# Kernel optimization log

Measured on AMD Instinct MI355X. Metric: run time of the kernel, lower is better.

Reference implementation:

```python
import jax, jax.numpy as jnp
import numpy as np

B, T, E, H, C = 64, 512, 768, 128, 18


def setup_inputs() -> dict:
    key = jax.random.key(0)
    ks = jax.random.split(key, 16)
    s = 1.0 / np.sqrt(H)
    inp = {
        "x": jax.random.normal(ks[0], (B, T, E), jnp.float32),
        "attention_mask": jnp.ones((B, T), jnp.int32),
        "labels": jax.random.randint(ks[1], (B, T), 0, C, jnp.int32),
        "Wih_f": jax.random.uniform(ks[2], (4 * H, E), jnp.float32, -s, s),
        "Whh_f": jax.random.uniform(ks[3], (4 * H, H), jnp.float32, -s, s),
        "b_f": jax.random.uniform(ks[4], (4 * H,), jnp.float32, -s, s),
        "Wih_b": jax.random.uniform(ks[5], (4 * H, E), jnp.float32, -s, s),
        "Whh_b": jax.random.uniform(ks[6], (4 * H, H), jnp.float32, -s, s),
        "b_b": jax.random.uniform(ks[7], (4 * H,), jnp.float32, -s, s),
        "Wfc": jax.random.uniform(ks[8], (C, 2 * H), jnp.float32, -s, s),
        "bfc": jax.random.uniform(ks[9], (C,), jnp.float32, -s, s),
        "start_trans": jax.random.normal(ks[10], (C,), jnp.float32) * 0.1,
        "end_trans": jax.random.normal(ks[11], (C,), jnp.float32) * 0.1,
        "trans": jax.random.normal(ks[12], (C, C), jnp.float32) * 0.1,
    }
    return inp


def _lstm_dir(x, Wih, Whh, b, reverse=False):
    # x: [B, T, E] -> hidden states [B, T, H]; torch LSTM gate order i,f,g,o
    if reverse:
        x = x[:, ::-1]
    pre = jnp.einsum("bte,ge->btg", x, Wih) + b  # [B, T, 4H] input projection once
    h0 = jnp.zeros((x.shape[0], H), x.dtype)

    def step(carry, pt):
        h, c = carry
        g = pt + h @ Whh.T
        i, f, gg, o = jnp.split(g, 4, axis=-1)
        c = jax.nn.sigmoid(f) * c + jax.nn.sigmoid(i) * jnp.tanh(gg)
        h = jax.nn.sigmoid(o) * jnp.tanh(c)
        return (h, c), h

    _, hs = jax.lax.scan(step, (h0, h0), jnp.swapaxes(pre, 0, 1))
    hs = jnp.swapaxes(hs, 0, 1)
    if reverse:
        hs = hs[:, ::-1]
    return hs


def _crf_loglik(em, tags, mask, start, end, trans):
    # pytorch-crf log-likelihood, batch_first. em [B,T,C], tags/mask [B,T]
    b, t, _ = em.shape
    maskf = mask.astype(em.dtype)
    tags = tags.astype(jnp.int32)
    # numerator: score of the given tag path
    em_sc = jnp.take_along_axis(em, tags[..., None], axis=2)[..., 0]  # [B,T]
    num = start[tags[:, 0]] + em_sc[:, 0]
    num = num + jnp.sum(em_sc[:, 1:] * maskf[:, 1:], axis=1)
    num = num + jnp.sum(trans[tags[:, :-1], tags[:, 1:]] * maskf[:, 1:], axis=1)
    last_idx = jnp.sum(mask.astype(jnp.int32), axis=1) - 1
    last_tags = jnp.take_along_axis(tags, last_idx[:, None], axis=1)[:, 0]
    num = num + end[last_tags]
    # denominator: forward algorithm (logsumexp recurrence over time)
    alpha0 = start + em[:, 0]  # [B,C]

    def step(alpha, inp):
        e_t, m_t = inp
        new = jax.scipy.special.logsumexp(alpha[:, :, None] + trans[None], axis=1) + e_t
        return jnp.where(m_t[:, None], new, alpha), None

    alpha, _ = jax.lax.scan(
        step, alpha0,
        (jnp.swapaxes(em[:, 1:], 0, 1), jnp.swapaxes(mask[:, 1:].astype(bool), 0, 1)),
    )
    den = jax.scipy.special.logsumexp(alpha + end, axis=1)
    return num - den


def _viterbi(em, start, end, trans):
    # em [B,T,C] -> best path [B,T] (full mask)
    s0 = start + em[:, 0]

    def fstep(score, e_t):
        cand = score[:, :, None] + trans[None]  # [B,C,C]
        return jnp.max(cand, axis=1) + e_t, jnp.argmax(cand, axis=1)

    score, bptr = jax.lax.scan(fstep, s0, jnp.swapaxes(em[:, 1:], 0, 1))  # bptr [T-1,B,C]
    last = jnp.argmax(score + end, axis=1)  # [B]

    def bstep(tag, ptr_t):
        prev = jnp.take_along_axis(ptr_t, tag[:, None], axis=1)[:, 0]
        return prev, prev

    _, path = jax.lax.scan(bstep, last, bptr, reverse=True)  # [T-1,B]
    return jnp.concatenate([jnp.swapaxes(path, 0, 1), last[:, None]], axis=1)


def reference(x, attention_mask, labels, Wih_f, Whh_f, b_f, Wih_b, Whh_b, b_b,
              Wfc, bfc, start_trans, end_trans, trans):
    hf = _lstm_dir(x, Wih_f, Whh_f, b_f, reverse=False)
    hb = _lstm_dir(x, Wih_b, Whh_b, b_b, reverse=True)
    seq = jnp.concatenate([hf, hb], axis=-1)  # [B,T,2H]
    em = seq @ Wfc.T + bfc  # [B,T,C] emissions
    mask = attention_mask.astype(bool)
    llh = _crf_loglik(em, labels, mask, start_trans, end_trans, trans)
    loss = -jnp.sum(llh) / x.shape[0]  # reduction='sum' then / batch_size
    path = _viterbi(em, start_trans, end_trans, trans) + 1  # res_paths = x+1
    return path, loss
```

## Files before the change

kernel.cpp:

```cpp
#include <hip/hip_runtime.h>
#include <hip/hip_bf16.h>
#include <math.h>

typedef __attribute__((ext_vector_type(8))) short short8;
typedef __attribute__((ext_vector_type(4))) float f32x4;

constexpr int nB = 64, nT = 512, nE = 768, nH = 128, nG = 512, nC = 18;
constexpr int nBT = nB * nT;

__device__ __forceinline__ float bf2f(unsigned short u) { return __uint_as_float(((unsigned int)u) << 16); }
__device__ __forceinline__ unsigned short f2bf(float f) {
  __hip_bfloat16 h = __float2bfloat16(f);
  return *reinterpret_cast<unsigned short*>(&h);
}
__device__ __forceinline__ float rlane(float v, int lane) {
  return __uint_as_float(__builtin_amdgcn_readlane(__float_as_uint(v), lane));
}
__device__ __forceinline__ float fast_sig(float x) {
  return __builtin_amdgcn_rcpf(1.0f + __builtin_amdgcn_exp2f(-1.44269504f * x));
}
__device__ __forceinline__ float fast_tanh(float x) {
  return 1.0f - 2.0f * __builtin_amdgcn_rcpf(1.0f + __builtin_amdgcn_exp2f(2.88539008f * x));
}
__device__ __forceinline__ float fast_exp(float x) { return __builtin_amdgcn_exp2f(1.44269504f * x); }
__device__ __forceinline__ float fast_log(float x) { return __builtin_amdgcn_logf(x) * 0.69314718f; }

__global__ __launch_bounds__(256) void cvt_kernel(const float* __restrict__ in,
                                                  unsigned short* __restrict__ out, int n8) {
  int i = blockIdx.x * blockDim.x + threadIdx.x;
  const int stride = gridDim.x * blockDim.x;
  for (; i < n8; i += stride) {
    const float4 a = ((const float4*)in)[(size_t)i * 2];
    const float4 b = ((const float4*)in)[(size_t)i * 2 + 1];
    unsigned short u[8] = {f2bf(a.x), f2bf(a.y), f2bf(a.z), f2bf(a.w),
                           f2bf(b.x), f2bf(b.y), f2bf(b.z), f2bf(b.w)};
    ((float4*)out)[i] = *(float4*)u;
  }
}

__global__ __launch_bounds__(256) void proj_kernel(
    const float* __restrict__ x,
    const unsigned short* __restrict__ wfb, const unsigned short* __restrict__ wbb,
    const float* __restrict__ biasF, const float* __restrict__ biasB,
    unsigned short* __restrict__ Pf, unsigned short* __restrict__ Pb)
{
  const int bid = blockIdx.x;
  const int mt = bid & 255, sub = bid >> 8;
  const int dir = sub >> 2, nt = sub & 3;
  const unsigned short* W = dir ? wbb : wfb;
  const float* bias = dir ? biasB : biasF;
  unsigned short* P = dir ? Pb : Pf;
  const int m0 = mt * 128, n0 = nt * 128;

  __shared__ unsigned short As[128 * 40];
  __shared__ unsigned short Bs[128 * 40];
  const int tid = threadIdx.x;
  const int w = tid >> 6, lane = tid & 63, l15 = lane & 15, l4 = lane >> 4;
  const int wr = w >> 1, wc = w & 1;
  const int srow = tid >> 1, shalf = tid & 1;

  const float* srcA = x + (size_t)(m0 + srow) * nE + shalf * 16;
  const unsigned short* srcB = W + (size_t)(n0 + srow) * nE + shalf * 16;

  f32x4 acc[4][4];
#pragma unroll
  for (int i = 0; i < 4; ++i)
#pragma unroll
    for (int j = 0; j < 4; ++j) acc[i][j] = (f32x4){0.f, 0.f, 0.f, 0.f};

  for (int k0 = 0; k0 < nE; k0 += 32) {
    const float4 a0 = *(const float4*)(srcA + k0);
    const float4 a1 = *(const float4*)(srcA + k0 + 4);
    const float4 a2 = *(const float4*)(srcA + k0 + 8);
    const float4 a3 = *(const float4*)(srcA + k0 + 12);
    const float4 b0 = *(const float4*)(srcB + k0);
    const float4 b1 = *(const float4*)(srcB + k0 + 8);
    unsigned short ua[16] = {f2bf(a0.x), f2bf(a0.y), f2bf(a0.z), f2bf(a0.w),
                             f2bf(a1.x), f2bf(a1.y), f2bf(a1.z), f2bf(a1.w),
                             f2bf(a2.x), f2bf(a2.y), f2bf(a2.z), f2bf(a2.w),
                             f2bf(a3.x), f2bf(a3.y), f2bf(a3.z), f2bf(a3.w)};
    __syncthreads();
    *(float4*)&As[srow * 40 + shalf * 16] = *(float4*)&ua[0];
    *(float4*)&As[srow * 40 + shalf * 16 + 8] = *(float4*)&ua[8];
    *(float4*)&Bs[srow * 40 + shalf * 16] = b0;
    *(float4*)&Bs[srow * 40 + shalf * 16 + 8] = b1;
    __syncthreads();
    short8 af[4], bfr[4];
#pragma unroll
    for (int i = 0; i < 4; ++i) af[i] = *(const short8*)&As[(wr * 64 + i * 16 + l15) * 40 + l4 * 8];
#pragma unroll
    for (int j = 0; j < 4; ++j) bfr[j] = *(const short8*)&Bs[(wc * 64 + j * 16 + l15) * 40 + l4 * 8];
#pragma unroll
    for (int i = 0; i < 4; ++i)
#pragma unroll
      for (int j = 0; j < 4; ++j)
        acc[i][j] = __builtin_amdgcn_mfma_f32_16x16x32_bf16(af[i], bfr[j], acc[i][j], 0, 0, 0);
  }
  float bv[4];
#pragma unroll
  for (int j = 0; j < 4; ++j) bv[j] = bias[n0 + wc * 64 + j * 16 + l15];
#pragma unroll
  for (int i = 0; i < 4; ++i) {
#pragma unroll
    for (int j = 0; j < 4; ++j) {
      const int col = n0 + wc * 64 + j * 16 + l15;
#pragma unroll
      for (int r = 0; r < 4; ++r) {
        const int row = m0 + wr * 64 + i * 16 + l4 * 4 + r;
        P[(size_t)row * nG + col] = f2bf(acc[i][j][r] + bv[j]);
      }
    }
  }
}

__global__ __launch_bounds__(512, 1) void lstm_kernel(
    const unsigned short* __restrict__ Pf, const unsigned short* __restrict__ Pb,
    const float* __restrict__ WhhF, const float* __restrict__ WhhB,
    unsigned short* __restrict__ hf, unsigned short* __restrict__ hb)
{
  const int bid = blockIdx.x;
  const int dir = bid & 1, grp = bid >> 1;
  const int b0 = grp * 4;
  const unsigned short* pre = dir ? Pb : Pf;
  const float* Whh = dir ? WhhB : WhhF;
  unsigned short* hout = dir ? hb : hf;

  const int tid = threadIdx.x, w = tid >> 6, lane = tid & 63;
  const int l15 = lane & 15, l4 = lane >> 4;
  const int batch = l15 & 3, msel = l15 >> 2;
  const int cell = w * 16 + msel * 4 + l4;
  const int swz = batch * 40;

  __shared__ unsigned short h_lds[2 * 4 * 128];

  short8 Af[4][4];
#pragma unroll
  for (int m = 0; m < 4; ++m) {
    const int gp = w * 64 + m * 16 + l15;
    const int gorig = (gp & 3) * 128 + (gp >> 2);
#pragma unroll
    for (int kk = 0; kk < 4; ++kk) {
      const float* wp = Whh + (size_t)gorig * nH + kk * 32 + l4 * 8;
      const float4 v0 = *(const float4*)wp;
      const float4 v1 = *(const float4*)(wp + 4);
      unsigned short u[8] = {f2bf(v0.x), f2bf(v0.y), f2bf(v0.z), f2bf(v0.w),
                             f2bf(v1.x), f2bf(v1.y), f2bf(v1.z), f2bf(v1.w)};
      Af[m][kk] = *(short8*)u;
    }
  }
  for (int i = tid; i < 2 * 4 * 128; i += 512) h_lds[i] = 0;

  float c_state = 0.f;
  const unsigned short* pbase = pre + (size_t)(b0 + batch) * nT * nG + cell;

  unsigned short pA[4], pB[4];
  {
    const int tt0 = dir ? (nT - 1) : 0;
    const int tt1 = dir ? (nT - 2) : 1;
#pragma unroll
    for (int r = 0; r < 4; ++r) pA[r] = pbase[(size_t)tt0 * nG + r * 128];
#pragma unroll
    for (int r = 0; r < 4; ++r) pB[r] = pbase[(size_t)tt1 * nG + r * 128];
  }
  __syncthreads();

#define LSTM_STEP(RB, T, BUFC)                                                   \
  {                                                                              \
    const int ttime = dir ? (nT - 1 - (T)) : (T);                                \
    float pg[4];                                                                 \
    _Pragma("unroll")                                                            \
    for (int r = 0; r < 4; ++r) pg[r] = bf2f(BUFC[r]);                           \
    {                                                                            \
      const int tl = ((T) + 2 < nT) ? (T) + 2 : (T);                             \
      const int ttl = dir ? (nT - 1 - tl) : tl;                                  \
      _Pragma("unroll")                                                          \
      for (int r = 0; r < 4; ++r) BUFC[r] = pbase[(size_t)ttl * nG + r * 128];   \
    }                                                                            \
    short8 bfr[4];                                                               \
    _Pragma("unroll")                                                            \
    for (int kk = 0; kk < 4; ++kk) {                                             \
      const int idx = (RB) * 512 + batch * 128 + ((kk * 32 + l4 * 8) ^ swz);     \
      bfr[kk] = *(const short8*)&h_lds[idx];                                     \
    }                                                                            \
    f32x4 acc[4];                                                                \
    _Pragma("unroll")                                                            \
    for (int m = 0; m < 4; ++m) acc[m] = (f32x4){0.f, 0.f, 0.f, 0.f};            \
    _Pragma("unroll")                                                            \
    for (int kk = 0; kk < 4; ++kk)                                               \
      _Pragma("unroll")                                                          \
      for (int m = 0; m < 4; ++m)                                                \
        acc[m] = __builtin_amdgcn_mfma_f32_16x16x32_bf16(Af[m][kk], bfr[kk], acc[m], 0, 0, 0); \
    const float g0 = msel < 2 ? (msel == 0 ? acc[0][0] : acc[1][0]) : (msel == 2 ? acc[2][0] : acc[3][0]); \
    const float g1 = msel < 2 ? (msel == 0 ? acc[0][1] : acc[1][1]) : (msel == 2 ? acc[2][1] : acc[3][1]); \
    const float g2 = msel < 2 ? (msel == 0 ? acc[0][2] : acc[1][2]) : (msel == 2 ? acc[2][2] : acc[3][2]); \
    const float g3 = msel < 2 ? (msel == 0 ? acc[0][3] : acc[1][3]) : (msel == 2 ? acc[2][3] : acc[3][3]); \
    const float gi = g0 + pg[0], gf = g1 + pg[1], gg = g2 + pg[2], go = g3 + pg[3]; \
    c_state = fast_sig(gf) * c_state + fast_sig(gi) * fast_tanh(gg);             \
    const float hval = fast_sig(go) * fast_tanh(c_state);                        \
    const unsigned short hu = f2bf(hval);                                        \
    h_lds[((RB) ^ 1) * 512 + batch * 128 + (cell ^ swz)] = hu;                   \
    hout[((size_t)(b0 + batch) * nT + ttime) * nH + cell] = hu;                  \
    asm volatile("s_waitcnt lgkmcnt(0)" ::: "memory");                           \
    __builtin_amdgcn_sched_barrier(0);                                           \
    __builtin_amdgcn_s_barrier();                                                \
  }

  for (int t2 = 0; t2 < nT; t2 += 2) {
    LSTM_STEP(0, t2, pA)
    LSTM_STEP(1, t2 + 1, pB)
  }
#undef LSTM_STEP
}

__global__ __launch_bounds__(256) void em_kernel(
    const unsigned short* __restrict__ hf, const unsigned short* __restrict__ hb,
    const float* __restrict__ Wfc, const float* __restrict__ bfc,
    float* __restrict__ em)
{
  __shared__ float seq[32][260];
  __shared__ float Wf[18][260];
  const int tid = threadIdx.x;
  const int row0 = blockIdx.x * 32;
  for (int i = tid; i < 32 * 32; i += 256) {
    const int r = i >> 5, seg = i & 31;
    const unsigned short* src = (seg < 16) ? (hf + (size_t)(row0 + r) * nH + seg * 8)
                                           : (hb + (size_t)(row0 + r) * nH + (seg - 16) * 8);
    const float4 v = *(const float4*)src;
    const unsigned short* u = (const unsigned short*)&v;
#pragma unroll
    for (int k = 0; k < 8; ++k) seq[r][seg * 8 + k] = bf2f(u[k]);
  }
  for (int i = tid; i < nC * 256; i += 256) {
    const int cc = i >> 8, k = i & 255;
    Wf[cc][k] = Wfc[cc * 256 + k];
  }
  __syncthreads();
  for (int o = tid; o < 32 * nC; o += 256) {
    const int r = o / nC, cc = o - r * nC;
    float acc = bfc[cc];
    const float4* s4 = (const float4*)&seq[r][0];
    const float4* w4 = (const float4*)&Wf[cc][0];
#pragma unroll
    for (int q = 0; q < 64; ++q) {
      const float4 a = s4[q]; const float4 wv = w4[q];
      acc += a.x * wv.x + a.y * wv.y + a.z * wv.z + a.w * wv.w;
    }
    em[(size_t)(row0 + r) * nC + cc] = acc;
  }
}

__global__ __launch_bounds__(128) void crfvit_kernel(
    const float* __restrict__ em, const int* __restrict__ labels,
    const int* __restrict__ mask, const float* __restrict__ start,
    const float* __restrict__ endt, const float* __restrict__ trans,
    float* __restrict__ llh, float* __restrict__ out_path)
{
  const int b = blockIdx.x; const int tid = threadIdx.x;
  __shared__ float tr[nC * nC];
  __shared__ unsigned char bp[(nT - 1) * nC];
  __shared__ unsigned char path[nT];
  for (int i = tid; i < nC * nC; i += 128) tr[i] = trans[i];
  __syncthreads();
  const float* eb = em + (size_t)b * nT * nC;

#define MAX18(c) fmaxf(fmaxf(fmaxf(fmaxf(fmaxf(c[0], c[1]), c[2]), fmaxf(fmaxf(c[3], c[4]), c[5])),           \
                             fmaxf(fmaxf(fmaxf(c[6], c[7]), c[8]), fmaxf(fmaxf(c[9], c[10]), c[11]))),        \
                       fmaxf(fmaxf(fmaxf(c[12], c[13]), c[14]), fmaxf(fmaxf(c[15], c[16]), c[17])))

  if (tid < 64) {
    const int l = tid;
    const int lc = l < nC ? l : nC - 1;
    const int* tg = labels + (size_t)b * nT;
    const int* mk = mask + (size_t)b * nT;

    float np = 0.f; int cnt = 0;
    for (int t = l; t < nT; t += 64) {
      const int tag = tg[t];
      const float e = eb[(size_t)t * nC + tag];
      if (t == 0) np += start[tag] + e;
      else np += (float)mk[t] * (e + tr[tg[t - 1] * nC + tag]);
      cnt += mk[t];
    }
#pragma unroll
    for (int off = 32; off; off >>= 1) { np += __shfl_xor(np, off); cnt += __shfl_xor(cnt, off); }
    const float num = np + endt[tg[cnt - 1]];

    float trc[nC];
#pragma unroll
    for (int i = 0; i < nC; ++i) trc[i] = tr[i * nC + lc];

    float alpha_r = start[lc] + eb[lc];
    float eA = eb[1 * nC + lc];
    float eB = eb[2 * nC + lc];
    float eC = eb[3 * nC + lc];
    for (int tk = 0; tk < 8; ++tk) {
      const unsigned long long mb = __ballot(mk[tk * 64 + l] != 0);
      for (int tt = (tk == 0 ? 1 : 0); tt < 64; ++tt) {
        const int t = tk * 64 + tt;
        const float ecur = eA; eA = eB; eB = eC;
        const int tl = t + 3 < nT ? t + 3 : nT - 1;
        eC = eb[(size_t)tl * nC + lc];
        float cand[nC];
#pragma unroll
        for (int i = 0; i < nC; ++i) cand[i] = rlane(alpha_r, i) + trc[i];
        const float m = MAX18(cand);
        float ex[nC];
#pragma unroll
        for (int i = 0; i < nC; ++i) ex[i] = fast_exp(cand[i] - m);
        float s = 0.f;
#pragma unroll
        for (int i = 0; i < nC; ++i) s += ex[i];
        const float anew = m + fast_log(s) + ecur;
        alpha_r = ((mb >> tt) & 1) ? anew : alpha_r;
      }
    }
    const float v = (l < nC) ? (alpha_r + endt[l]) : -3.0e38f;
    float m = v;
#pragma unroll
    for (int off = 32; off; off >>= 1) m = fmaxf(m, __shfl_xor(m, off));
    float s = (l < nC) ? fast_exp(v - m) : 0.f;
#pragma unroll
    for (int off = 32; off; off >>= 1) s += __shfl_xor(s, off);
    if (l == 0) llh[b] = num - (m + fast_log(s));
  } else {
    const int l = tid - 64;
    const int lc = l < nC ? l : nC - 1;
    float trc[nC];
#pragma unroll
    for (int i = 0; i < nC; ++i) trc[i] = tr[i * nC + lc];

    float score_r = start[lc] + eb[lc];
    float eA = eb[1 * nC + lc];
    float eB = eb[2 * nC + lc];
    float eC = eb[3 * nC + lc];
    for (int t = 1; t < nT; ++t) {
      const float ecur = eA; eA = eB; eB = eC;
      const int tl = t + 3 < nT ? t + 3 : nT - 1;
      eC = eb[(size_t)tl * nC + lc];
      float cand[nC];
#pragma unroll
      for (int i = 0; i < nC; ++i) cand[i] = rlane(score_r, i) + trc[i];
      const float m = MAX18(cand);
      int sel[nC];
#pragma unroll
      for (int i = 0; i < nC; ++i) sel[i] = (cand[i] == m) ? i : 63;
      int arg = sel[0];
#pragma unroll
      for (int i = 1; i < nC; ++i) arg = min(arg, sel[i]);
      score_r = m + ecur;
      if (l < nC) bp[(t - 1) * nC + l] = (unsigned char)arg;
    }
    if (l == 0) {
      float mm = -3.0e38f; int last = 0;
      for (int i = 0; i < nC; ++i) {
        const float v = rlane(score_r, i) + endt[i];
        if (v > mm) { mm = v; last = i; }
      }
      path[nT - 1] = (unsigned char)last;
      int cur = last;
      for (int t = nT - 2; t >= 0; --t) { cur = bp[t * nC + cur]; path[t] = (unsigned char)cur; }
    }
    asm volatile("s_waitcnt lgkmcnt(0)" ::: "memory");
    __builtin_amdgcn_wave_barrier();
    for (int t = l; t < nT; t += 64) out_path[(size_t)b * nT + t] = (float)(path[t] + 1);
  }
#undef MAX18
}

__global__ __launch_bounds__(64) void loss_kernel(const float* __restrict__ llh, float* __restrict__ out)
{
  const int l = threadIdx.x;
  float v = llh[l];
#pragma unroll
  for (int off = 32; off; off >>= 1) v += __shfl_xor(v, off);
  if (l == 0) out[0] = -v / (float)nB;
}

extern "C" void kernel_launch(void* const* d_in, const int* in_sizes, int n_in,
                              void* d_out, int out_size, void* d_ws, size_t ws_size,
                              hipStream_t stream)
{
  const float* x      = (const float*)d_in[0];
  const int*   amask  = (const int*)d_in[1];
  const int*   labels = (const int*)d_in[2];
  const float* Wih_f  = (const float*)d_in[3];
  const float* Whh_f  = (const float*)d_in[4];
  const float* b_f    = (const float*)d_in[5];
  const float* Wih_b  = (const float*)d_in[6];
  const float* Whh_b  = (const float*)d_in[7];
  const float* b_b    = (const float*)d_in[8];
  const float* Wfc    = (const float*)d_in[9];
  const float* bfc    = (const float*)d_in[10];
  const float* start  = (const float*)d_in[11];
  const float* endt   = (const float*)d_in[12];
  const float* trans  = (const float*)d_in[13];

  float* out = (float*)d_out;
  float* ws = (float*)d_ws;
  unsigned short* preF = (unsigned short*)ws;
  unsigned short* preB = preF + (size_t)nBT * nG;
  unsigned short* hf   = preB + (size_t)nBT * nG;
  unsigned short* hb   = hf + (size_t)nBT * nH;
  float* em  = (float*)(hb + (size_t)nBT * nH);
  float* llh = em + (size_t)nBT * nC;
  unsigned short* wfb = (unsigned short*)(llh + 64);
  unsigned short* wbb = wfb + (size_t)nG * nE;

  cvt_kernel<<<192, 256, 0, stream>>>(Wih_f, wfb, nG * nE / 8);
  cvt_kernel<<<192, 256, 0, stream>>>(Wih_b, wbb, nG * nE / 8);
  proj_kernel<<<2048, 256, 0, stream>>>(x, wfb, wbb, b_f, b_b, preF, preB);
  lstm_kernel<<<32, 512, 0, stream>>>(preF, preB, Whh_f, Whh_b, hf, hb);
  em_kernel<<<1024, 256, 0, stream>>>(hf, hb, Wfc, bfc, em);
  crfvit_kernel<<<64, 128, 0, stream>>>(em, labels, amask, start, endt, trans, llh, out);
  loss_kernel<<<1, 64, 0, stream>>>(llh, out + nBT);
}
```

Measured before the change: 549.0 us.

## Pre-convert x to bf16, merge weight casts, split CRF/Viterbi into separate blocks

Adds a separate pass that converts x to bf16 once, so the projection GEMM loads bf16 directly and no longer does per-tile float-to-bf16 conversion. The two weight-conversion launches are merged into one. The CRF forward and Viterbi passes now run as separate 64-thread blocks instead of two waves in one block, which doubles the block count. The CRF pass works in base-2 units with tree sums, and both passes prefetch emissions in unrolled chunks of 8. In exchange, the standalone x conversion adds a full extra read and write of x.

```diff
diff --git a/kernel.cpp b/kernel.cpp
--- a/kernel.cpp
+++ b/kernel.cpp
@@ -22,8 +22,6 @@
 __device__ __forceinline__ float fast_tanh(float x) {
   return 1.0f - 2.0f * __builtin_amdgcn_rcpf(1.0f + __builtin_amdgcn_exp2f(2.88539008f * x));
 }
-__device__ __forceinline__ float fast_exp(float x) { return __builtin_amdgcn_exp2f(1.44269504f * x); }
-__device__ __forceinline__ float fast_log(float x) { return __builtin_amdgcn_logf(x) * 0.69314718f; }
 
 __global__ __launch_bounds__(256) void cvt_kernel(const float* __restrict__ in,
                                                   unsigned short* __restrict__ out, int n8) {
@@ -38,8 +36,27 @@
   }
 }
 
+__global__ __launch_bounds__(256) void cvtw_kernel(const float* __restrict__ inF,
+                                                   const float* __restrict__ inB,
+                                                   unsigned short* __restrict__ outF,
+                                                   unsigned short* __restrict__ outB, int n8) {
+  const int half = gridDim.x >> 1;
+  const float* in = (blockIdx.x < half) ? inF : inB;
+  unsigned short* out = (blockIdx.x < half) ? outF : outB;
+  const int bid = (blockIdx.x < half) ? blockIdx.x : blockIdx.x - half;
+  int i = bid * blockDim.x + threadIdx.x;
+  const int stride = half * blockDim.x;
+  for (; i < n8; i += stride) {
+    const float4 a = ((const float4*)in)[(size_t)i * 2];
+    const float4 b = ((const float4*)in)[(size_t)i * 2 + 1];
+    unsigned short u[8] = {f2bf(a.x), f2bf(a.y), f2bf(a.z), f2bf(a.w),
+                           f2bf(b.x), f2bf(b.y), f2bf(b.z), f2bf(b.w)};
+    ((float4*)out)[i] = *(float4*)u;
+  }
+}
+
 __global__ __launch_bounds__(256) void proj_kernel(
-    const float* __restrict__ x,
+    const unsigned short* __restrict__ xbf,
     const unsigned short* __restrict__ wfb, const unsigned short* __restrict__ wbb,
     const float* __restrict__ biasF, const float* __restrict__ biasB,
     unsigned short* __restrict__ Pf, unsigned short* __restrict__ Pb)
@@ -59,7 +76,7 @@
   const int wr = w >> 1, wc = w & 1;
   const int srow = tid >> 1, shalf = tid & 1;
 
-  const float* srcA = x + (size_t)(m0 + srow) * nE + shalf * 16;
+  const unsigned short* srcA = xbf + (size_t)(m0 + srow) * nE + shalf * 16;
   const unsigned short* srcB = W + (size_t)(n0 + srow) * nE + shalf * 16;
 
   f32x4 acc[4][4];
@@ -70,18 +87,12 @@
 
   for (int k0 = 0; k0 < nE; k0 += 32) {
     const float4 a0 = *(const float4*)(srcA + k0);
-    const float4 a1 = *(const float4*)(srcA + k0 + 4);
-    const float4 a2 = *(const float4*)(srcA + k0 + 8);
-    const float4 a3 = *(const float4*)(srcA + k0 + 12);
+    const float4 a1 = *(const float4*)(srcA + k0 + 8);
     const float4 b0 = *(const float4*)(srcB + k0);
     const float4 b1 = *(const float4*)(srcB + k0 + 8);
-    unsigned short ua[16] = {f2bf(a0.x), f2bf(a0.y), f2bf(a0.z), f2bf(a0.w),
-                             f2bf(a1.x), f2bf(a1.y), f2bf(a1.z), f2bf(a1.w),
-                             f2bf(a2.x), f2bf(a2.y), f2bf(a2.z), f2bf(a2.w),
-                             f2bf(a3.x), f2bf(a3.y), f2bf(a3.z), f2bf(a3.w)};
     __syncthreads();
-    *(float4*)&As[srow * 40 + shalf * 16] = *(float4*)&ua[0];
-    *(float4*)&As[srow * 40 + shalf * 16 + 8] = *(float4*)&ua[8];
+    *(float4*)&As[srow * 40 + shalf * 16] = a0;
+    *(float4*)&As[srow * 40 + shalf * 16 + 8] = a1;
     *(float4*)&Bs[srow * 40 + shalf * 16] = b0;
     *(float4*)&Bs[srow * 40 + shalf * 16 + 8] = b1;
     __syncthreads();
@@ -249,27 +260,36 @@
   }
 }
 
-__global__ __launch_bounds__(128) void crfvit_kernel(
+__global__ __launch_bounds__(64) void crfvit_kernel(
     const float* __restrict__ em, const int* __restrict__ labels,
     const int* __restrict__ mask, const float* __restrict__ start,
     const float* __restrict__ endt, const float* __restrict__ trans,
     float* __restrict__ llh, float* __restrict__ out_path)
 {
-  const int b = blockIdx.x; const int tid = threadIdx.x;
+  constexpr float K2 = 1.44269504088896f;
+  constexpr float LN2 = 0.69314718055995f;
+  const int b = blockIdx.x >> 1, role = blockIdx.x & 1;
+  const int l = threadIdx.x;
   __shared__ float tr[nC * nC];
   __shared__ unsigned char bp[(nT - 1) * nC];
   __shared__ unsigned char path[nT];
-  for (int i = tid; i < nC * nC; i += 128) tr[i] = trans[i];
+  for (int i = l; i < nC * nC; i += 64) tr[i] = trans[i];
   __syncthreads();
   const float* eb = em + (size_t)b * nT * nC;
+  const int lc = l < nC ? l : nC - 1;
 
 #define MAX18(c) fmaxf(fmaxf(fmaxf(fmaxf(fmaxf(c[0], c[1]), c[2]), fmaxf(fmaxf(c[3], c[4]), c[5])),           \
                              fmaxf(fmaxf(fmaxf(c[6], c[7]), c[8]), fmaxf(fmaxf(c[9], c[10]), c[11]))),        \
                        fmaxf(fmaxf(fmaxf(c[12], c[13]), c[14]), fmaxf(fmaxf(c[15], c[16]), c[17])))
-
-  if (tid < 64) {
-    const int l = tid;
-    const int lc = l < nC ? l : nC - 1;
+#define TREESUM(ex, s) {                                                          \
+    const float p0 = ex[0] + ex[1], p1 = ex[2] + ex[3], p2 = ex[4] + ex[5];       \
+    const float p3 = ex[6] + ex[7], p4 = ex[8] + ex[9], p5 = ex[10] + ex[11];     \
+    const float p6 = ex[12] + ex[13], p7 = ex[14] + ex[15], p8 = ex[16] + ex[17]; \
+    const float q0 = p0 + p1, q1 = p2 + p3, q2 = p4 + p5, q3 = p6 + p7;           \
+    s = ((q0 + q1) + (q2 + q3)) + p8;                                             \
+  }
+
+  if (role == 0) {
     const int* tg = labels + (size_t)b * nT;
     const int* mk = mask + (size_t)b * nT;
 
@@ -287,69 +307,89 @@
 
     float trc[nC];
 #pragma unroll
+    for (int i = 0; i < nC; ++i) trc[i] = tr[i * nC + lc] * K2;
+
+    float alpha2 = (start[lc] + eb[lc]) * K2;
+    float ec[8], en[8];
+#pragma unroll
+    for (int j = 0; j < 8; ++j) ec[j] = eb[j * nC + lc] * K2;
+#pragma unroll
+    for (int j = 0; j < 8; ++j) en[j] = eb[(8 + j) * nC + lc] * K2;
+    unsigned long long mb = __ballot(mk[l] != 0);
+
+#define CRF_STEP(T, E) {                                                          \
+      float cand[nC];                                                             \
+      _Pragma("unroll")                                                           \
+      for (int i = 0; i < nC; ++i) cand[i] = rlane(alpha2, i) + trc[i];           \
+      const float m = MAX18(cand);                                                \
+      float ex[nC];                                                               \
+      _Pragma("unroll")                                                           \
+      for (int i = 0; i < nC; ++i) ex[i] = __builtin_amdgcn_exp2f(cand[i] - m);   \
+      float s; TREESUM(ex, s);                                                    \
+      const float anew = m + __builtin_amdgcn_logf(s) + (E);                      \
+      alpha2 = ((mb >> ((T) & 63)) & 1) ? anew : alpha2;                          \
+    }
+
+#pragma unroll
+    for (int j = 1; j < 8; ++j) CRF_STEP(j, ec[j])
+    for (int c = 1; c < 64; ++c) {
+#pragma unroll
+      for (int j = 0; j < 8; ++j) ec[j] = en[j];
+      const int tn = (c < 63) ? (c + 1) * 8 : 504;
+#pragma unroll
+      for (int j = 0; j < 8; ++j) en[j] = eb[(size_t)(tn + j) * nC + lc] * K2;
+      if ((c & 7) == 0) mb = __ballot(mk[c * 8 + l] != 0);
+#pragma unroll
+      for (int j = 0; j < 8; ++j) CRF_STEP(c * 8 + j, ec[j])
+    }
+#undef CRF_STEP
+    const float v = (l < nC) ? (alpha2 + endt[l] * K2) : -3.0e38f;
+    float m = v;
+#pragma unroll
+    for (int off = 32; off; off >>= 1) m = fmaxf(m, __shfl_xor(m, off));
+    float s = (l < nC) ? __builtin_amdgcn_exp2f(v - m) : 0.f;
+#pragma unroll
+    for (int off = 32; off; off >>= 1) s += __shfl_xor(s, off);
+    if (l == 0) llh[b] = num - (m + __builtin_amdgcn_logf(s)) * LN2;
+  } else {
+    float trc[nC];
+#pragma unroll
     for (int i = 0; i < nC; ++i) trc[i] = tr[i * nC + lc];
 
-    float alpha_r = start[lc] + eb[lc];
-    float eA = eb[1 * nC + lc];
-    float eB = eb[2 * nC + lc];
-    float eC = eb[3 * nC + lc];
-    for (int tk = 0; tk < 8; ++tk) {
-      const unsigned long long mb = __ballot(mk[tk * 64 + l] != 0);
-      for (int tt = (tk == 0 ? 1 : 0); tt < 64; ++tt) {
-        const int t = tk * 64 + tt;
-        const float ecur = eA; eA = eB; eB = eC;
-        const int tl = t + 3 < nT ? t + 3 : nT - 1;
-        eC = eb[(size_t)tl * nC + lc];
-        float cand[nC];
-#pragma unroll
-        for (int i = 0; i < nC; ++i) cand[i] = rlane(alpha_r, i) + trc[i];
-        const float m = MAX18(cand);
-        float ex[nC];
-#pragma unroll
-        for (int i = 0; i < nC; ++i) ex[i] = fast_exp(cand[i] - m);
-        float s = 0.f;
-#pragma unroll
-        for (int i = 0; i < nC; ++i) s += ex[i];
-        const float anew = m + fast_log(s) + ecur;
-        alpha_r = ((mb >> tt) & 1) ? anew : alpha_r;
-      }
-    }
-    const float v = (l < nC) ? (alpha_r + endt[l]) : -3.0e38f;
-    float m = v;
-#pragma unroll
-    for (int off = 32; off; off >>= 1) m = fmaxf(m, __shfl_xor(m, off));
-    float s = (l < nC) ? fast_exp(v - m) : 0.f;
-#pragma unroll
-    for (int off = 32; off; off >>= 1) s += __shfl_xor(s, off);
-    if (l == 0) llh[b] = num - (m + fast_log(s));
-  } else {
-    const int l = tid - 64;
-    const int lc = l < nC ? l : nC - 1;
-    float trc[nC];
-#pragma unroll
-    for (int i = 0; i < nC; ++i) trc[i] = tr[i * nC + lc];
-
     float score_r = start[lc] + eb[lc];
-    float eA = eb[1 * nC + lc];
-    float eB = eb[2 * nC + lc];
-    float eC = eb[3 * nC + lc];
-    for (int t = 1; t < nT; ++t) {
-      const float ecur = eA; eA = eB; eB = eC;
-      const int tl = t + 3 < nT ? t + 3 : nT - 1;
-      eC = eb[(size_t)tl * nC + lc];
-      float cand[nC];
-#pragma unroll
-      for (int i = 0; i < nC; ++i) cand[i] = rlane(score_r, i) + trc[i];
-      const float m = MAX18(cand);
-      int sel[nC];
-#pragma unroll
-      for (int i = 0; i < nC; ++i) sel[i] = (cand[i] == m) ? i : 63;
-      int arg = sel[0];
-#pragma unroll
-      for (int i = 1; i < nC; ++i) arg = min(arg, sel[i]);
-      score_r = m + ecur;
-      if (l < nC) bp[(t - 1) * nC + l] = (unsigned char)arg;
-    }
+    float ec[8], en[8];
+#pragma unroll
+    for (int j = 0; j < 8; ++j) ec[j] = eb[j * nC + lc];
+#pragma unroll
+    for (int j = 0; j < 8; ++j) en[j] = eb[(8 + j) * nC + lc];
+
+#define VIT_STEP(T, E) {                                                          \
+      float cand[nC];                                                             \
+      _Pragma("unroll")                                                           \
+      for (int i = 0; i < nC; ++i) cand[i] = rlane(score_r, i) + trc[i];          \
+      const float m = MAX18(cand);                                                \
+      int sel[nC];                                                                \
+      _Pragma("unroll")                                                           \
+      for (int i = 0; i < nC; ++i) sel[i] = (cand[i] == m) ? i : 63;              \
+      int arg = sel[0];                                                           \
+      _Pragma("unroll")                                                           \
+      for (int i = 1; i < nC; ++i) arg = min(arg, sel[i]);                        \
+      score_r = m + (E);                                                          \
+      if (l < nC) bp[((T) - 1) * nC + l] = (unsigned char)arg;                    \
+    }
+
+#pragma unroll
+    for (int j = 1; j < 8; ++j) VIT_STEP(j, ec[j])
+    for (int c = 1; c < 64; ++c) {
+#pragma unroll
+      for (int j = 0; j < 8; ++j) ec[j] = en[j];
+      const int tn = (c < 63) ? (c + 1) * 8 : 504;
+#pragma unroll
+      for (int j = 0; j < 8; ++j) en[j] = eb[(size_t)(tn + j) * nC + lc];
+#pragma unroll
+      for (int j = 0; j < 8; ++j) VIT_STEP(c * 8 + j, ec[j])
+    }
+#undef VIT_STEP
     if (l == 0) {
       float mm = -3.0e38f; int last = 0;
       for (int i = 0; i < nC; ++i) {
@@ -365,6 +405,7 @@
     for (int t = l; t < nT; t += 64) out_path[(size_t)b * nT + t] = (float)(path[t] + 1);
   }
 #undef MAX18
+#undef TREESUM
 }
 
 __global__ __launch_bounds__(64) void loss_kernel(const float* __restrict__ llh, float* __restrict__ out)
@@ -403,14 +444,15 @@
   unsigned short* hb   = hf + (size_t)nBT * nH;
   float* em  = (float*)(hb + (size_t)nBT * nH);
   float* llh = em + (size_t)nBT * nC;
-  unsigned short* wfb = (unsigned short*)(llh + 64);
+  unsigned short* xbf = (unsigned short*)(llh + 64);
+  unsigned short* wfb = xbf + (size_t)nBT * nE;
   unsigned short* wbb = wfb + (size_t)nG * nE;
 
-  cvt_kernel<<<192, 256, 0, stream>>>(Wih_f, wfb, nG * nE / 8);
-  cvt_kernel<<<192, 256, 0, stream>>>(Wih_b, wbb, nG * nE / 8);
-  proj_kernel<<<2048, 256, 0, stream>>>(x, wfb, wbb, b_f, b_b, preF, preB);
+  cvt_kernel<<<4096, 256, 0, stream>>>(x, xbf, nBT * nE / 8);
+  cvtw_kernel<<<384, 256, 0, stream>>>(Wih_f, Wih_b, wfb, wbb, nG * nE / 8);
+  proj_kernel<<<2048, 256, 0, stream>>>(xbf, wfb, wbb, b_f, b_b, preF, preB);
   lstm_kernel<<<32, 512, 0, stream>>>(preF, preB, Whh_f, Whh_b, hf, hb);
   em_kernel<<<1024, 256, 0, stream>>>(hf, hb, Wfc, bfc, em);
-  crfvit_kernel<<<64, 128, 0, stream>>>(em, labels, amask, start, endt, trans, llh, out);
+  crfvit_kernel<<<128, 64, 0, stream>>>(em, labels, amask, start, endt, trans, llh, out);
   loss_kernel<<<1, 64, 0, stream>>>(llh, out + nBT);
 }
```

Result: no change. 542.4 us (-1.2%).
